# Kernel tuning notes

Measured on AMD Instinct MI355X. Metric: run time of the kernel, lower is better.

The kernel has to match this reference:

```python
import math
import jax, jax.numpy as jnp
import numpy as np

B, D, CTX, HID, NSTEPS = 16384, 16, 256, 192, 10
IN_DIM = D + CTX + 1  # 273
DT = -0.1  # integrate t: 1 -> 0 in 10 fixed RK4 steps


def setup_inputs() -> dict:
    key = jax.random.key(0)
    ks = jax.random.split(key, 9)
    rn = lambda k, shape, sc=1.0: jax.random.normal(k, shape, dtype=jnp.float32) * sc
    return {
        "theta": rn(ks[0], (B, D)),
        "h": rn(ks[1], (B, CTX)),
        "eps": rn(ks[2], (NSTEPS, 4, B, D)),  # fresh Hutchinson noise per RK4 stage
        "W1": rn(ks[3], (IN_DIM, HID), 0.5 / np.sqrt(IN_DIM)),
        "b1": jnp.zeros((HID,), jnp.float32),
        "W2": rn(ks[4], (HID, HID), 0.5 / np.sqrt(HID)),
        "b2": jnp.zeros((HID,), jnp.float32),
        "W3": rn(ks[5], (HID, D), 0.5 / np.sqrt(HID)),
        "b3": jnp.zeros((D,), jnp.float32),
    }


def _mlp(x, W1, b1, W2, b2, W3, b3):
    # CNF_MLP depth=2: Linear->GELU->Linear->GELU->Linear (exact erf GELU, torch default)
    h1 = jax.nn.gelu(x @ W1 + b1, approximate=False)
    h2 = jax.nn.gelu(h1 @ W2 + b2, approximate=False)
    return h2 @ W3 + b3


def reference(theta, h, eps, W1, b1, W2, b2, W3, b3):
    """ConditionalCNF.log_prob: RK4 (torchdiffeq 3/8 variant) from t=1 to t=0
    with Hutchinson trace estimator via JVP (eps^T J eps)."""
    dt = jnp.float32(DT)

    def vf(t, y, e):
        def net(y_):
            tf = jnp.full((y_.shape[0], 1), t, y_.dtype)
            return _mlp(jnp.concatenate([y_, h, tf], axis=1), W1, b1, W2, b2, W3, b3)
        f, Je = jax.jvp(net, (y,), (e,))  # Je = J @ e
        trace = jnp.sum(e * Je, axis=1)   # eps^T J eps == (J^T eps) . eps
        return f, -trace

    def step(carry, xs):
        y, logp = carry
        t, e4 = xs  # e4: (4, B, D)
        f1, l1 = vf(t, y, e4[0])
        f2, l2 = vf(t + dt / 3, y + dt * f1 / 3, e4[1])
        f3, l3 = vf(t + 2 * dt / 3, y + dt * (f2 - f1 / 3), e4[2])
        f4, l4 = vf(t + dt, y + dt * (f1 - f2 + f3), e4[3])
        y2 = y + dt * (f1 + 3 * (f2 + f3) + f4) * 0.125
        lp2 = logp + dt * (l1 + 3 * (l2 + l3) + l4) * 0.125
        return (y2, lp2), None

    ts = jnp.float32(1.0) + dt * jnp.arange(NSTEPS, dtype=jnp.float32)
    logp0 = jnp.zeros((theta.shape[0],), theta.dtype)
    (z0, dlogp), _ = jax.lax.scan(step, (theta, logp0), (ts, eps))
    base = -0.5 * jnp.sum(z0 ** 2, axis=1) - 0.5 * D * math.log(2 * math.pi)
    return base - dlogp
```

## Files before the change

kernel.cpp:

```cpp
#include <hip/hip_runtime.h>
#include <math.h>


#define DTc (-0.1f)

typedef __attribute__((ext_vector_type(8))) short bf16x8;
typedef __attribute__((ext_vector_type(8))) unsigned short u16x8;
typedef __attribute__((ext_vector_type(4))) float f32x4;

#define MFMA16(a, b, c) __builtin_amdgcn_mfma_f32_16x16x32_bf16((a), (b), (c), 0, 0, 0)

__device__ __forceinline__ unsigned short f2bf(float x) {
    union { float f; unsigned int u; } c; c.f = x;
    unsigned int r = c.u + 0x7FFFu + ((c.u >> 16) & 1u);
    return (unsigned short)(r >> 16);
}

__device__ __forceinline__ unsigned int pk2bf(float lo, float hi) {
#if __has_builtin(__builtin_amdgcn_cvt_pk_bf16_f32)
    auto v = __builtin_amdgcn_cvt_pk_bf16_f32(lo, hi);
    return __builtin_bit_cast(unsigned int, v);
#else
    return (unsigned int)f2bf(lo) | ((unsigned int)f2bf(hi) << 16);
#endif
}

__device__ __forceinline__ void gelu_both(float x, float& gv, float& dv) {
    float z  = fabsf(x) * 0.70710678118654752f;
    float e  = __builtin_amdgcn_exp2f(x * x * -0.72134752044448170f);
    float t  = __builtin_amdgcn_rcpf(__builtin_fmaf(0.47047f, z, 1.0f));
    float p  = t * (0.1740121f + t * (-0.0479399f + t * 0.3739278f));
    float ch = p * e;
    float cdf = (x >= 0.0f) ? (1.0f - ch) : ch;
    gv = x * cdf;
    dv = __builtin_fmaf(0.39894228040143268f * x, e, cdf);
}

__global__ void repack_kernel(const float* __restrict__ W1, const float* __restrict__ W2,
                              const float* __restrict__ W3,
                              unsigned short* __restrict__ w2f, unsigned short* __restrict__ w1yf,
                              unsigned short* __restrict__ w1cf, unsigned short* __restrict__ w3fg) {
    int t = blockIdx.x * 256 + threadIdx.x;
    u16x8 v;
    if (t < 4608) {
        int kb = t / 768, rem = t % 768, nt = rem / 64, lane = rem % 64;
        int n = nt * 16 + (lane & 15), k0 = kb * 32 + (lane >> 4) * 8;
        #pragma unroll
        for (int j = 0; j < 8; ++j) v[j] = f2bf(W2[(k0 + j) * 192 + n]);
        *(u16x8*)(w2f + t * 8) = v;
    } else if (t < 5376) {
        int i2 = t - 4608, nt = i2 / 64, lane = i2 % 64;
        int n = nt * 16 + (lane & 15), k0 = (lane >> 4) * 8;
        #pragma unroll
        for (int j = 0; j < 8; ++j) {
            int k = k0 + j;
            v[j] = (k < 16) ? f2bf(W1[k * 192 + n])
                 : (k == 16) ? f2bf(W1[272 * 192 + n]) : (unsigned short)0;
        }
        *(u16x8*)(w1yf + i2 * 8) = v;
    } else if (t < 11520) {
        int i3 = t - 5376, kb = i3 / 768, rem = i3 % 768, nt = rem / 64, lane = rem % 64;
        int n = nt * 16 + (lane & 15), k0 = kb * 32 + (lane >> 4) * 8;
        #pragma unroll
        for (int j = 0; j < 8; ++j) v[j] = f2bf(W1[(16 + k0 + j) * 192 + n]);
        *(u16x8*)(w1cf + i3 * 8) = v;
    } else if (t < 11904) {
        int i4 = t - 11520, kb = i4 / 64, lane = i4 % 64;
        int n = lane & 15, k0 = kb * 32 + (lane >> 4) * 8;
        #pragma unroll
        for (int j = 0; j < 8; ++j) v[j] = f2bf(W3[(k0 + j) * 16 + n]);
        *(u16x8*)(w3fg + i4 * 8) = v;
    }
}

__global__ __launch_bounds__(256, 2) void cnf_mfma(
    const float* __restrict__ theta, const float* __restrict__ hctx,
    const float* __restrict__ eps,   const float* __restrict__ b1,
    const float* __restrict__ b2,    const float* __restrict__ b3,
    const unsigned short* __restrict__ w2f, const unsigned short* __restrict__ w1yf,
    const unsigned short* __restrict__ w1cf, const unsigned short* __restrict__ w3fg,
    float* __restrict__ out)
{
    __shared__ __align__(16) unsigned short Ys[64 * 24];
    __shared__ __align__(16) unsigned short Xa0[64 * 200];
    __shared__ __align__(16) unsigned short Xa1[64 * 200];
    __shared__ __align__(16) float ebf[2][512];
    __shared__ float trx[32];

    const int tid  = threadIdx.x;
    const int wave = tid >> 6, lane = tid & 63;
    const int l15  = lane & 15, quad = lane >> 4;
    const int r0   = blockIdx.x * 32;
    const int ntg0 = wave * 3;

    unsigned short* Hs = Xa0;
    for (int t4 = tid; t4 < 2048; t4 += 256) {
        int r = t4 >> 6, k = (t4 & 63) * 4;
        float4 v = *(const float4*)(hctx + (long)(r0 + r) * 256 + k);
        *(uint2*)(&Hs[r * 264 + k]) = make_uint2(pk2bf(v.x, v.y), pk2bf(v.z, v.w));
    }

    const int  ek = ((wave - 2) * 64 + lane) * 4;
    const int  er = ek >> 4, ed = ek & 15;
    const long epsBase = (long)r0 * 16 + ek;
    float4 epr;
    if (wave >= 2) epr = *(const float4*)(eps + epsBase);

    bf16x8 b1yfr[3], w3fr[6];
    #pragma unroll
    for (int nt = 0; nt < 3; ++nt)
        b1yfr[nt] = *reinterpret_cast<const bf16x8*>(w1yf + ((ntg0 + nt) * 64 + lane) * 8);
    #pragma unroll
    for (int kb = 0; kb < 6; ++kb)
        w3fr[kb] = *reinterpret_cast<const bf16x8*>(w3fg + (kb * 64 + lane) * 8);
    float b2r[3], b1r[3];
    #pragma unroll
    for (int nt = 0; nt < 3; ++nt) {
        int n = (ntg0 + nt) * 16 + l15;
        b2r[nt] = b2[n];
        b1r[nt] = b1[n];
    }
    const float b3r = b3[l15];

    float yreg[2][4];
    if (wave == 0) {
        #pragma unroll
        for (int mt = 0; mt < 2; ++mt)
            #pragma unroll
            for (int i = 0; i < 4; ++i)
                yreg[mt][i] = theta[(r0 + mt * 16 + quad * 4 + i) * 16 + l15];
    }

    __syncthreads();

    float cr[2][3][4];
    {
        f32x4 ca[2][3] = {};
        #pragma unroll
        for (int kb = 0; kb < 8; ++kb) {
            bf16x8 af[2];
            #pragma unroll
            for (int mt = 0; mt < 2; ++mt)
                af[mt] = *reinterpret_cast<const bf16x8*>(&Hs[(mt * 16 + l15) * 264 + kb * 32 + quad * 8]);
            #pragma unroll
            for (int nt = 0; nt < 3; ++nt) {
                bf16x8 bf = *reinterpret_cast<const bf16x8*>(w1cf + ((kb * 12 + ntg0 + nt) * 64 + lane) * 8);
                #pragma unroll
                for (int mt = 0; mt < 2; ++mt)
                    ca[mt][nt] = MFMA16(af[mt], bf, ca[mt][nt]);
            }
        }
        #pragma unroll
        for (int mt = 0; mt < 2; ++mt)
            #pragma unroll
            for (int nt = 0; nt < 3; ++nt)
                #pragma unroll
                for (int i = 0; i < 4; ++i)
                    cr[mt][nt][i] = ca[mt][nt][i] + b1r[nt];
    }

    if (wave == 0) {
        #pragma unroll
        for (int mt = 0; mt < 2; ++mt)
            #pragma unroll
            for (int i = 0; i < 4; ++i)
                Ys[(mt * 16 + quad * 4 + i) * 24 + l15] = f2bf(yreg[mt][i]);
    }
    if (wave >= 2) {
        *(uint2*)(&Ys[(32 + er) * 24 + ed]) = make_uint2(pk2bf(epr.x, epr.y), pk2bf(epr.z, epr.w));
        *(float4*)(&ebf[0][ek]) = epr;
        epr = *(const float4*)(eps + (long)1 * 262144 + epsBase);
    }

    float F1[2][4], F2[2][4], F3[2][4];
    float tracc[2][4] = {{0.f,0.f,0.f,0.f},{0.f,0.f,0.f,0.f}};

    for (int sg = 0; sg < 40; ++sg) {
        const int sub = sg & 3;
        const float ts = 1.0f + DTc * (float)(sg >> 2) + DTc * ((float)sub * (1.0f / 3.0f));
        const short tsb = (short)f2bf(ts);

        __syncthreads();

        {
            bf16x8 af[4];
            if (quad < 2) {
                #pragma unroll
                for (int mt = 0; mt < 4; ++mt)
                    af[mt] = *reinterpret_cast<const bf16x8*>(&Ys[(mt * 16 + l15) * 24 + quad * 8]);
            } else {
                #pragma unroll
                for (int mt = 0; mt < 4; ++mt) af[mt] = bf16x8{};
                if (quad == 2) { af[0][0] = tsb; af[1][0] = tsb; }
            }
            f32x4 acc[4][3] = {};
            #pragma unroll
            for (int nt = 0; nt < 3; ++nt)
                #pragma unroll
                for (int mt = 0; mt < 4; ++mt)
                    acc[mt][nt] = MFMA16(af[mt], b1yfr[nt], acc[mt][nt]);
            #pragma unroll
            for (int nt = 0; nt < 3; ++nt) {
                int n = (ntg0 + nt) * 16 + l15;
                #pragma unroll
                for (int mt = 0; mt < 2; ++mt) {
                    float gvv[4], dvv[4];
                    #pragma unroll
                    for (int i = 0; i < 4; ++i) {
                        float a = acc[mt][nt][i] + cr[mt][nt][i];
                        float gv, dv; gelu_both(a, gv, dv);
                        gvv[i] = gv; dvv[i] = dv * acc[mt + 2][nt][i];
                    }
                    unsigned int p0 = pk2bf(gvv[0], gvv[1]), p1 = pk2bf(gvv[2], gvv[3]);
                    unsigned int q0 = pk2bf(dvv[0], dvv[1]), q1 = pk2bf(dvv[2], dvv[3]);
                    int ba = (mt * 16 + quad * 4) * 200 + n;
                    Xa0[ba]          = (unsigned short)p0;
                    Xa0[ba + 200]    = (unsigned short)(p0 >> 16);
                    Xa0[ba + 400]    = (unsigned short)p1;
                    Xa0[ba + 600]    = (unsigned short)(p1 >> 16);
                    Xa0[ba + 6400]   = (unsigned short)q0;
                    Xa0[ba + 6600]   = (unsigned short)(q0 >> 16);
                    Xa0[ba + 6800]   = (unsigned short)q1;
                    Xa0[ba + 7000]   = (unsigned short)(q1 >> 16);
                }
            }
        }
        __syncthreads();

        {
            f32x4 acc2[4][3] = {};
            #pragma unroll
            for (int kb = 0; kb < 6; ++kb) {
                bf16x8 aA[4];
                #pragma unroll
                for (int mt = 0; mt < 4; ++mt)
                    aA[mt] = *reinterpret_cast<const bf16x8*>(&Xa0[(mt * 16 + l15) * 200 + kb * 32 + quad * 8]);
                #pragma unroll
                for (int nt = 0; nt < 3; ++nt) {
                    bf16x8 bf = *reinterpret_cast<const bf16x8*>(w2f + ((kb * 12 + ntg0 + nt) * 64 + lane) * 8);
                    #pragma unroll
                    for (int mt = 0; mt < 4; ++mt)
                        acc2[mt][nt] = MFMA16(aA[mt], bf, acc2[mt][nt]);
                }
            }
            #pragma unroll
            for (int nt = 0; nt < 3; ++nt) {
                int n = (ntg0 + nt) * 16 + l15;
                #pragma unroll
                for (int mt = 0; mt < 2; ++mt) {
                    float gvv[4], dvv[4];
                    #pragma unroll
                    for (int i = 0; i < 4; ++i) {
                        float a = acc2[mt][nt][i] + b2r[nt];
                        float gv, dv; gelu_both(a, gv, dv);
                        gvv[i] = gv; dvv[i] = dv * acc2[mt + 2][nt][i];
                    }
                    unsigned int p0 = pk2bf(gvv[0], gvv[1]), p1 = pk2bf(gvv[2], gvv[3]);
                    unsigned int q0 = pk2bf(dvv[0], dvv[1]), q1 = pk2bf(dvv[2], dvv[3]);
                    int ba = (mt * 16 + quad * 4) * 200 + n;
                    Xa1[ba]          = (unsigned short)p0;
                    Xa1[ba + 200]    = (unsigned short)(p0 >> 16);
                    Xa1[ba + 400]    = (unsigned short)p1;
                    Xa1[ba + 600]    = (unsigned short)(p1 >> 16);
                    Xa1[ba + 6400]   = (unsigned short)q0;
                    Xa1[ba + 6600]   = (unsigned short)(q0 >> 16);
                    Xa1[ba + 6800]   = (unsigned short)q1;
                    Xa1[ba + 7000]   = (unsigned short)(q1 >> 16);
                }
            }
        }
        __syncthreads();

        if (wave < 2) {
            f32x4 acc3[2] = {};
            #pragma unroll
            for (int kb = 0; kb < 6; ++kb)
                #pragma unroll
                for (int mt = 0; mt < 2; ++mt) {
                    bf16x8 af = *reinterpret_cast<const bf16x8*>(
                        &Xa1[(wave * 32 + mt * 16 + l15) * 200 + kb * 32 + quad * 8]);
                    acc3[mt] = MFMA16(af, w3fr[kb], acc3[mt]);
                }

            if (wave == 0) {
                float Fc[2][4];
                #pragma unroll
                for (int mt = 0; mt < 2; ++mt)
                    #pragma unroll
                    for (int i = 0; i < 4; ++i) Fc[mt][i] = acc3[mt][i] + b3r;
                if (sub == 0) {
                    #pragma unroll
                    for (int mt = 0; mt < 2; ++mt)
                        for (int i = 0; i < 4; ++i) F1[mt][i] = Fc[mt][i];
                } else if (sub == 1) {
                    #pragma unroll
                    for (int mt = 0; mt < 2; ++mt)
                        for (int i = 0; i < 4; ++i) F2[mt][i] = Fc[mt][i];
                } else if (sub == 2) {
                    #pragma unroll
                    for (int mt = 0; mt < 2; ++mt)
                        for (int i = 0; i < 4; ++i) F3[mt][i] = Fc[mt][i];
                } else {
                    #pragma unroll
                    for (int mt = 0; mt < 2; ++mt)
                        #pragma unroll
                        for (int i = 0; i < 4; ++i)
                            yreg[mt][i] += DTc * 0.125f *
                                (F1[mt][i] + 3.0f * (F2[mt][i] + F3[mt][i]) + Fc[mt][i]);
                }
                if (sg < 39) {
                    const int sub2 = (sg + 1) & 3;
                    #pragma unroll
                    for (int mt = 0; mt < 2; ++mt)
                        #pragma unroll
                        for (int i = 0; i < 4; ++i) {
                            float ys = yreg[mt][i];
                            if (sub2 == 1)      ys += DTc * (1.0f / 3.0f) * F1[mt][i];
                            else if (sub2 == 2) ys += DTc * (F2[mt][i] - (1.0f / 3.0f) * F1[mt][i]);
                            else if (sub2 == 3) ys += DTc * (F1[mt][i] - F2[mt][i] + F3[mt][i]);
                            Ys[(mt * 16 + quad * 4 + i) * 24 + l15] = f2bf(ys);
                        }
                }
            } else {
                const float csub = (sub == 1 || sub == 2) ? 3.0f : 1.0f;
                #pragma unroll
                for (int mt = 0; mt < 2; ++mt)
                    #pragma unroll
                    for (int i = 0; i < 4; ++i) {
                        int r = mt * 16 + quad * 4 + i;
                        float p = ebf[sg & 1][r * 16 + l15] * acc3[mt][i];
                        p += __shfl_xor(p, 1);
                        p += __shfl_xor(p, 2);
                        p += __shfl_xor(p, 4);
                        p += __shfl_xor(p, 8);
                        tracc[mt][i] += csub * p;
                    }
            }
        } else {
            if (sg < 39) {
                *(uint2*)(&Ys[(32 + er) * 24 + ed]) = make_uint2(pk2bf(epr.x, epr.y), pk2bf(epr.z, epr.w));
                *(float4*)(&ebf[(sg + 1) & 1][ek]) = epr;
                if (sg < 38)
                    epr = *(const float4*)(eps + (long)(sg + 2) * 262144 + epsBase);
            }
        }
    }

    if (wave == 1 && l15 == 0) {
        #pragma unroll
        for (int mt = 0; mt < 2; ++mt)
            #pragma unroll
            for (int i = 0; i < 4; ++i) trx[mt * 16 + quad * 4 + i] = tracc[mt][i];
    }
    __syncthreads();
    if (wave == 0) {
        #pragma unroll
        for (int mt = 0; mt < 2; ++mt)
            #pragma unroll
            for (int i = 0; i < 4; ++i) {
                float q = yreg[mt][i] * yreg[mt][i];
                q += __shfl_xor(q, 1);
                q += __shfl_xor(q, 2);
                q += __shfl_xor(q, 4);
                q += __shfl_xor(q, 8);
                if (l15 == 0)
                    out[r0 + mt * 16 + quad * 4 + i] =
                        -0.5f * q - 14.7030165313f + DTc * 0.125f * trx[mt * 16 + quad * 4 + i];
            }
    }
}

extern "C" void kernel_launch(void* const* d_in, const int* in_sizes, int n_in,
                              void* d_out, int out_size, void* d_ws, size_t ws_size,
                              hipStream_t stream) {
    const float* theta = (const float*)d_in[0];
    const float* hctx  = (const float*)d_in[1];
    const float* eps   = (const float*)d_in[2];
    const float* W1    = (const float*)d_in[3];
    const float* b1    = (const float*)d_in[4];
    const float* W2    = (const float*)d_in[5];
    const float* b2    = (const float*)d_in[6];
    const float* W3    = (const float*)d_in[7];
    const float* b3    = (const float*)d_in[8];
    float* outp = (float*)d_out;

    unsigned short* w2f  = (unsigned short*)d_ws;
    unsigned short* w1yf = w2f + 36864;
    unsigned short* w1cf = w1yf + 6144;
    unsigned short* w3fg = w1cf + 49152;

    hipLaunchKernelGGL(repack_kernel, dim3(47), dim3(256), 0, stream,
                       W1, W2, W3, w2f, w1yf, w1cf, w3fg);
    hipLaunchKernelGGL(cnf_mfma, dim3(512), dim3(256), 0, stream,
                       theta, hctx, eps, b1, b2, b3, w2f, w1yf, w1cf, w3fg, outp);
}
```

Before: 381.0 us.

## Spread layer-3 and RK4 update across all four waves, fold biases into accumulators

Before, only waves 0-1 ran the final W3 GEMM, each handling two 16-row tiles, and the trace shuffle reduction ran on every stage. Now all four waves each do one 16-row tile: waves 0-1 handle the primal rows and the RK4 state update, waves 2-3 handle the tangent rows and the trace accumulation. The trace is accumulated per lane with an FMA and reduced only once at the end instead of per stage. The bias terms b1/ctx and b2/b3 are preloaded into the MFMA accumulators, which removes the separate adds. This shortens the serial tail of each stage and the cross-lane shuffles, at the cost of moving the state to different waves and changing the FP summation order of the trace.

```diff
diff --git a/kernel.cpp b/kernel.cpp
--- a/kernel.cpp
+++ b/kernel.cpp
@@ -92,6 +92,7 @@
     const int l15  = lane & 15, quad = lane >> 4;
     const int r0   = blockIdx.x * 32;
     const int ntg0 = wave * 3;
+    const int mtw  = wave & 1;
 
     unsigned short* Hs = Xa0;
     for (int t4 = tid; t4 < 2048; t4 += 256) {
@@ -122,13 +123,11 @@
     }
     const float b3r = b3[l15];
 
-    float yreg[2][4];
-    if (wave == 0) {
-        #pragma unroll
-        for (int mt = 0; mt < 2; ++mt)
-            #pragma unroll
-            for (int i = 0; i < 4; ++i)
-                yreg[mt][i] = theta[(r0 + mt * 16 + quad * 4 + i) * 16 + l15];
+    float yreg[4];
+    if (wave < 2) {
+        #pragma unroll
+        for (int i = 0; i < 4; ++i)
+            yreg[i] = theta[(r0 + mtw * 16 + quad * 4 + i) * 16 + l15];
     }
 
     __syncthreads();
@@ -159,12 +158,10 @@
                     cr[mt][nt][i] = ca[mt][nt][i] + b1r[nt];
     }
 
-    if (wave == 0) {
-        #pragma unroll
-        for (int mt = 0; mt < 2; ++mt)
-            #pragma unroll
-            for (int i = 0; i < 4; ++i)
-                Ys[(mt * 16 + quad * 4 + i) * 24 + l15] = f2bf(yreg[mt][i]);
+    if (wave < 2) {
+        #pragma unroll
+        for (int i = 0; i < 4; ++i)
+            Ys[(mtw * 16 + quad * 4 + i) * 24 + l15] = f2bf(yreg[i]);
     }
     if (wave >= 2) {
         *(uint2*)(&Ys[(32 + er) * 24 + ed]) = make_uint2(pk2bf(epr.x, epr.y), pk2bf(epr.z, epr.w));
@@ -172,8 +169,8 @@
         epr = *(const float4*)(eps + (long)1 * 262144 + epsBase);
     }
 
-    float F1[2][4], F2[2][4], F3[2][4];
-    float tracc[2][4] = {{0.f,0.f,0.f,0.f},{0.f,0.f,0.f,0.f}};
+    float F1[4], F2[4], F3[4];
+    float tracc[4] = {0.f, 0.f, 0.f, 0.f};
 
     for (int sg = 0; sg < 40; ++sg) {
         const int sub = sg & 3;
@@ -193,7 +190,15 @@
                 for (int mt = 0; mt < 4; ++mt) af[mt] = bf16x8{};
                 if (quad == 2) { af[0][0] = tsb; af[1][0] = tsb; }
             }
-            f32x4 acc[4][3] = {};
+            f32x4 acc[4][3];
+            #pragma unroll
+            for (int nt = 0; nt < 3; ++nt) {
+                #pragma unroll
+                for (int mt = 0; mt < 2; ++mt)
+                    acc[mt][nt] = f32x4{cr[mt][nt][0], cr[mt][nt][1], cr[mt][nt][2], cr[mt][nt][3]};
+                acc[2][nt] = f32x4{};
+                acc[3][nt] = f32x4{};
+            }
             #pragma unroll
             for (int nt = 0; nt < 3; ++nt)
                 #pragma unroll
@@ -207,8 +212,7 @@
                     float gvv[4], dvv[4];
                     #pragma unroll
                     for (int i = 0; i < 4; ++i) {
-                        float a = acc[mt][nt][i] + cr[mt][nt][i];
-                        float gv, dv; gelu_both(a, gv, dv);
+                        float gv, dv; gelu_both(acc[mt][nt][i], gv, dv);
                         gvv[i] = gv; dvv[i] = dv * acc[mt + 2][nt][i];
                     }
                     unsigned int p0 = pk2bf(gvv[0], gvv[1]), p1 = pk2bf(gvv[2], gvv[3]);
@@ -228,7 +232,14 @@
         __syncthreads();
 
         {
-            f32x4 acc2[4][3] = {};
+            f32x4 acc2[4][3];
+            #pragma unroll
+            for (int nt = 0; nt < 3; ++nt) {
+                acc2[0][nt] = f32x4{b2r[nt], b2r[nt], b2r[nt], b2r[nt]};
+                acc2[1][nt] = acc2[0][nt];
+                acc2[2][nt] = f32x4{};
+                acc2[3][nt] = f32x4{};
+            }
             #pragma unroll
             for (int kb = 0; kb < 6; ++kb) {
                 bf16x8 aA[4];
@@ -251,8 +262,7 @@
                     float gvv[4], dvv[4];
                     #pragma unroll
                     for (int i = 0; i < 4; ++i) {
-                        float a = acc2[mt][nt][i] + b2r[nt];
-                        float gv, dv; gelu_both(a, gv, dv);
+                        float gv, dv; gelu_both(acc2[mt][nt][i], gv, dv);
                         gvv[i] = gv; dvv[i] = dv * acc2[mt + 2][nt][i];
                     }
                     unsigned int p0 = pk2bf(gvv[0], gvv[1]), p1 = pk2bf(gvv[2], gvv[3]);
@@ -271,102 +281,82 @@
         }
         __syncthreads();
 
-        if (wave < 2) {
-            f32x4 acc3[2] = {};
+        {
+            f32x4 acc3 = (wave < 2) ? f32x4{b3r, b3r, b3r, b3r} : f32x4{};
+            const unsigned short* src = &Xa1[(wave * 16 + l15) * 200];
             #pragma unroll
             for (int kb = 0; kb < 6; ++kb)
-                #pragma unroll
-                for (int mt = 0; mt < 2; ++mt) {
-                    bf16x8 af = *reinterpret_cast<const bf16x8*>(
-                        &Xa1[(wave * 32 + mt * 16 + l15) * 200 + kb * 32 + quad * 8]);
-                    acc3[mt] = MFMA16(af, w3fr[kb], acc3[mt]);
-                }
-
-            if (wave == 0) {
-                float Fc[2][4];
-                #pragma unroll
-                for (int mt = 0; mt < 2; ++mt)
-                    #pragma unroll
-                    for (int i = 0; i < 4; ++i) Fc[mt][i] = acc3[mt][i] + b3r;
+                acc3 = MFMA16(*reinterpret_cast<const bf16x8*>(src + kb * 32 + quad * 8), w3fr[kb], acc3);
+
+            if (wave < 2) {
                 if (sub == 0) {
                     #pragma unroll
-                    for (int mt = 0; mt < 2; ++mt)
-                        for (int i = 0; i < 4; ++i) F1[mt][i] = Fc[mt][i];
+                    for (int i = 0; i < 4; ++i) F1[i] = acc3[i];
                 } else if (sub == 1) {
                     #pragma unroll
-                    for (int mt = 0; mt < 2; ++mt)
-                        for (int i = 0; i < 4; ++i) F2[mt][i] = Fc[mt][i];
+                    for (int i = 0; i < 4; ++i) F2[i] = acc3[i];
                 } else if (sub == 2) {
                     #pragma unroll
-                    for (int mt = 0; mt < 2; ++mt)
-                        for (int i = 0; i < 4; ++i) F3[mt][i] = Fc[mt][i];
+                    for (int i = 0; i < 4; ++i) F3[i] = acc3[i];
                 } else {
                     #pragma unroll
-                    for (int mt = 0; mt < 2; ++mt)
-                        #pragma unroll
-                        for (int i = 0; i < 4; ++i)
-                            yreg[mt][i] += DTc * 0.125f *
-                                (F1[mt][i] + 3.0f * (F2[mt][i] + F3[mt][i]) + Fc[mt][i]);
+                    for (int i = 0; i < 4; ++i)
+                        yreg[i] += DTc * 0.125f * (F1[i] + 3.0f * (F2[i] + F3[i]) + acc3[i]);
                 }
                 if (sg < 39) {
                     const int sub2 = (sg + 1) & 3;
                     #pragma unroll
-                    for (int mt = 0; mt < 2; ++mt)
-                        #pragma unroll
-                        for (int i = 0; i < 4; ++i) {
-                            float ys = yreg[mt][i];
-                            if (sub2 == 1)      ys += DTc * (1.0f / 3.0f) * F1[mt][i];
-                            else if (sub2 == 2) ys += DTc * (F2[mt][i] - (1.0f / 3.0f) * F1[mt][i]);
-                            else if (sub2 == 3) ys += DTc * (F1[mt][i] - F2[mt][i] + F3[mt][i]);
-                            Ys[(mt * 16 + quad * 4 + i) * 24 + l15] = f2bf(ys);
-                        }
+                    for (int i = 0; i < 4; ++i) {
+                        float ys = yreg[i];
+                        if (sub2 == 1)      ys += DTc * (1.0f / 3.0f) * F1[i];
+                        else if (sub2 == 2) ys += DTc * (F2[i] - (1.0f / 3.0f) * F1[i]);
+                        else if (sub2 == 3) ys += DTc * (F1[i] - F2[i] + F3[i]);
+                        Ys[(mtw * 16 + quad * 4 + i) * 24 + l15] = f2bf(ys);
+                    }
                 }
             } else {
                 const float csub = (sub == 1 || sub == 2) ? 3.0f : 1.0f;
                 #pragma unroll
-                for (int mt = 0; mt < 2; ++mt)
-                    #pragma unroll
-                    for (int i = 0; i < 4; ++i) {
-                        int r = mt * 16 + quad * 4 + i;
-                        float p = ebf[sg & 1][r * 16 + l15] * acc3[mt][i];
-                        p += __shfl_xor(p, 1);
-                        p += __shfl_xor(p, 2);
-                        p += __shfl_xor(p, 4);
-                        p += __shfl_xor(p, 8);
-                        tracc[mt][i] += csub * p;
-                    }
-            }
-        } else {
-            if (sg < 39) {
-                *(uint2*)(&Ys[(32 + er) * 24 + ed]) = make_uint2(pk2bf(epr.x, epr.y), pk2bf(epr.z, epr.w));
-                *(float4*)(&ebf[(sg + 1) & 1][ek]) = epr;
-                if (sg < 38)
-                    epr = *(const float4*)(eps + (long)(sg + 2) * 262144 + epsBase);
-            }
-        }
-    }
-
-    if (wave == 1 && l15 == 0) {
-        #pragma unroll
-        for (int mt = 0; mt < 2; ++mt)
-            #pragma unroll
-            for (int i = 0; i < 4; ++i) trx[mt * 16 + quad * 4 + i] = tracc[mt][i];
+                for (int i = 0; i < 4; ++i) {
+                    int r = mtw * 16 + quad * 4 + i;
+                    tracc[i] = __builtin_fmaf(csub * ebf[sg & 1][r * 16 + l15], acc3[i], tracc[i]);
+                }
+                if (sg < 39) {
+                    *(uint2*)(&Ys[(32 + er) * 24 + ed]) = make_uint2(pk2bf(epr.x, epr.y), pk2bf(epr.z, epr.w));
+                    *(float4*)(&ebf[(sg + 1) & 1][ek]) = epr;
+                    if (sg < 38)
+                        epr = *(const float4*)(eps + (long)(sg + 2) * 262144 + epsBase);
+                }
+            }
+        }
+    }
+
+    if (wave >= 2) {
+        #pragma unroll
+        for (int i = 0; i < 4; ++i) {
+            float v = tracc[i];
+            v += __shfl_xor(v, 1);
+            v += __shfl_xor(v, 2);
+            v += __shfl_xor(v, 4);
+            v += __shfl_xor(v, 8);
+            if (l15 == 0) trx[mtw * 16 + quad * 4 + i] = v;
+        }
     }
     __syncthreads();
-    if (wave == 0) {
-        #pragma unroll
-        for (int mt = 0; mt < 2; ++mt)
-            #pragma unroll
-            for (int i = 0; i < 4; ++i) {
-                float q = yreg[mt][i] * yreg[mt][i];
-                q += __shfl_xor(q, 1);
-                q += __shfl_xor(q, 2);
-                q += __shfl_xor(q, 4);
-                q += __shfl_xor(q, 8);
-                if (l15 == 0)
-                    out[r0 + mt * 16 + quad * 4 + i] =
-                        -0.5f * q - 14.7030165313f + DTc * 0.125f * trx[mt * 16 + quad * 4 + i];
-            }
+
+    if (wave < 2) {
+        #pragma unroll
+        for (int i = 0; i < 4; ++i) {
+            float q = yreg[i] * yreg[i];
+            q += __shfl_xor(q, 1);
+            q += __shfl_xor(q, 2);
+            q += __shfl_xor(q, 4);
+            q += __shfl_xor(q, 8);
+            if (l15 == 0) {
+                int r = mtw * 16 + quad * 4 + i;
+                out[r0 + r] = -0.5f * q - 14.7030165313f + DTc * 0.125f * trx[r];
+            }
+        }
     }
 }
 
```

New measurement: 347.1 us. 1.1x faster.
